# Optimization experiments

Measured on AMD Instinct MI355X. Metric: run time of the kernel, lower is better.

The kernel has to match this reference:

```python
import jax, jax.numpy as jnp
import numpy as np

BS, C_IN, CTX, TGT = 2, 8, 1024, 96
D_MODEL, N_HEADS, D_FF, N_LAYERS = 256, 16, 1024, 4
PF, SF, PC, SC = 8, 4, 32, 16
NF = (CTX + SF - PF) // SF + 1   # 256 fine patches (incl. end-pad)
NC = (CTX + SC - PC) // SC + 1   # 64 coarse patches
TOTAL = NF + NC                  # 320
EPS = 1e-5
DK = D_MODEL // N_HEADS
SCALE = DK ** -0.5


def _patchify(z, plen, stride):
    # ReplicationPad1d((0, stride)) then unfold -> (bs, c, n_patches, plen)
    pad = jnp.broadcast_to(z[..., -1:], z.shape[:-1] + (stride,))
    zp = jnp.concatenate([z, pad], axis=-1)
    n = (zp.shape[-1] - plen) // stride + 1
    idx = np.arange(n)[:, None] * stride + np.arange(plen)[None, :]
    return zp[..., idx]


def _layernorm(x, s, b):
    m = x.mean(-1, keepdims=True)
    v = jnp.var(x, axis=-1, keepdims=True)
    return (x - m) * jax.lax.rsqrt(v + EPS) * s + b


def setup_inputs() -> dict:
    key = jax.random.key(0)
    ks = jax.random.split(key, 16)
    g = lambda k, shape: jax.random.normal(k, shape, jnp.float32) * 0.02
    return {
        "z": jax.random.normal(ks[0], (BS, C_IN, CTX), jnp.float32),
        "revin_w": jnp.ones((C_IN,), jnp.float32),
        "revin_b": jnp.zeros((C_IN,), jnp.float32),
        "Wf": g(ks[1], (PF, D_MODEL)), "bf": jnp.zeros((D_MODEL,), jnp.float32),
        "Wc": g(ks[2], (PC, D_MODEL)), "bc": jnp.zeros((D_MODEL,), jnp.float32),
        "W_pos": jax.random.uniform(ks[3], (TOTAL, D_MODEL), jnp.float32, -0.02, 0.02),
        "WQ": g(ks[4], (N_LAYERS, D_MODEL, D_MODEL)), "bQ": jnp.zeros((N_LAYERS, D_MODEL), jnp.float32),
        "WK": g(ks[5], (N_LAYERS, D_MODEL, D_MODEL)), "bK": jnp.zeros((N_LAYERS, D_MODEL), jnp.float32),
        "WV": g(ks[6], (N_LAYERS, D_MODEL, D_MODEL)), "bV": jnp.zeros((N_LAYERS, D_MODEL), jnp.float32),
        "WO": g(ks[7], (N_LAYERS, D_MODEL, D_MODEL)), "bO": jnp.zeros((N_LAYERS, D_MODEL), jnp.float32),
        "ln1_s": jnp.ones((N_LAYERS, D_MODEL), jnp.float32), "ln1_b": jnp.zeros((N_LAYERS, D_MODEL), jnp.float32),
        "ln2_s": jnp.ones((N_LAYERS, D_MODEL), jnp.float32), "ln2_b": jnp.zeros((N_LAYERS, D_MODEL), jnp.float32),
        "F1": g(ks[8], (N_LAYERS, D_MODEL, D_FF)), "c1": jnp.zeros((N_LAYERS, D_FF), jnp.float32),
        "F2": g(ks[9], (N_LAYERS, D_FF, D_MODEL)), "c2": jnp.zeros((N_LAYERS, D_MODEL), jnp.float32),
        "Wh": g(ks[10], (D_MODEL * TOTAL, TGT)), "bh": jnp.zeros((TGT,), jnp.float32),
    }


def reference(z, revin_w, revin_b, Wf, bf, Wc, bc, W_pos, WQ, bQ, WK, bK, WV, bV,
              WO, bO, ln1_s, ln1_b, ln2_s, ln2_b, F1, c1, F2, c2, Wh, bh):
    # RevIN norm over the time axis (last axis of (bs, c, T))
    mean = z.mean(-1, keepdims=True)
    std = jnp.sqrt(jnp.var(z, axis=-1, keepdims=True) + EPS)
    zn = (z - mean) / std * revin_w[None, :, None] + revin_b[None, :, None]

    # dual-scale patch embedding
    x_fine = _patchify(zn, PF, SF) @ Wf + bf      # (bs, c, NF, d)
    x_coarse = _patchify(zn, PC, SC) @ Wc + bc    # (bs, c, NC, d)
    x = jnp.concatenate([x_fine, x_coarse], axis=2)  # (bs, c, TOTAL, d)

    u = x.reshape(BS * C_IN, TOTAL, D_MODEL) + W_pos  # (B, S, d), B=bs*c

    # residual-score transformer encoder (post-norm)
    prev = None
    for l in range(N_LAYERS):
        q = (u @ WQ[l] + bQ[l]).reshape(-1, TOTAL, N_HEADS, DK).transpose(0, 2, 1, 3)
        k = (u @ WK[l] + bK[l]).reshape(-1, TOTAL, N_HEADS, DK).transpose(0, 2, 1, 3)
        v = (u @ WV[l] + bV[l]).reshape(-1, TOTAL, N_HEADS, DK).transpose(0, 2, 1, 3)
        s = jnp.einsum('bhqd,bhkd->bhqk', q, k) * SCALE
        if prev is not None:
            s = s + prev
        w = jax.nn.softmax(s, axis=-1)
        o = jnp.einsum('bhqk,bhkd->bhqd', w, v).transpose(0, 2, 1, 3).reshape(-1, TOTAL, D_MODEL)
        o = o @ WO[l] + bO[l]
        u = _layernorm(u + o, ln1_s[l], ln1_b[l])
        h = jax.nn.gelu(u @ F1[l] + c1[l], approximate=False) @ F2[l] + c2[l]
        u = _layernorm(u + h, ln2_s[l], ln2_b[l])
        prev = s

    # head: (bs, c, TOTAL, d) -> permute -> flatten(d, TOTAL) -> linear
    zz = u.reshape(BS, C_IN, TOTAL, D_MODEL).transpose(0, 1, 3, 2).reshape(BS, C_IN, D_MODEL * TOTAL)
    out = zz @ Wh + bh  # (bs, c, TGT)

    # RevIN denorm
    out = (out - revin_b[None, :, None]) / (revin_w[None, :, None] + EPS * EPS) * std + mean
    return out
```

## Files before the change

kernel.cpp:

```cpp
#include <hip/hip_runtime.h>
#include <math.h>

typedef unsigned short ushort;
typedef unsigned int uint;
typedef __attribute__((ext_vector_type(8))) short short8;
typedef __attribute__((ext_vector_type(4))) float f32x4;
typedef __attribute__((ext_vector_type(4))) ushort us4;

constexpr int BS = 2, C_IN = 8, CTX = 1024, TGT = 96;
constexpr int DM = 256, NH = 16, DFF = 1024, NL = 4;
constexpr int NF = 256, TOTAL = 320;
constexpr int NB = 16;
constexpr int DK = 16;
constexpr float EPS = 1e-5f;
constexpr float SCALE = 0.25f;
constexpr int KHEAD = DM * TOTAL;
constexpr int M = NB * TOTAL;

__device__ __forceinline__ ushort f2b(float x) {
    uint u = __float_as_uint(x);
    u += 0x7fff + ((u >> 16) & 1);
    return (ushort)(u >> 16);
}
__device__ __forceinline__ float bu2f(ushort x) { return __uint_as_float(((uint)x) << 16); }
__device__ __forceinline__ uint pack2(float a, float b) { return (uint)f2b(a) | ((uint)f2b(b) << 16); }

typedef __attribute__((address_space(3))) uint lds_u32;
typedef const __attribute__((address_space(1))) uint glb_u32;
__device__ __forceinline__ void ldst16(const void* g, void* l) {
    __builtin_amdgcn_global_load_lds((glb_u32*)g, (lds_u32*)l, 16, 0, 0);
}

#define PIPE_BARRIER() asm volatile("s_waitcnt vmcnt(0)\n\ts_barrier" ::: "memory")

__global__ __launch_bounds__(256) void k_prep(
        const float* __restrict__ WQ, const float* __restrict__ WK,
        const float* __restrict__ WV, const float* __restrict__ WO,
        const float* __restrict__ F1, const float* __restrict__ F2,
        const float* __restrict__ Wh,
        ushort* __restrict__ Wtqkv, ushort* __restrict__ WtO,
        ushort* __restrict__ Ft1, ushort* __restrict__ Ft2,
        ushort* __restrict__ WhT2,
        const float* __restrict__ z, const float* __restrict__ rw,
        const float* __restrict__ rb,
        const float* __restrict__ Wf, const float* __restrict__ bfv,
        const float* __restrict__ Wc, const float* __restrict__ bcv,
        const float* __restrict__ Wpos, ushort* __restrict__ u,
        const float* __restrict__ bhv, float* __restrict__ outp,
        float* __restrict__ scalef) {
    __shared__ __align__(16) ushort tile[64 * 98];
    __shared__ float szn[CTX];
    __shared__ float red1[4], red2[4];
    int i = blockIdx.x, tid = threadIdx.x;

    if (i < 768) {
        const float* src; ushort* dst; int lsrc, ldst_, r0, c0;
        if (i < 256) {
            int mat = i >> 4, l = mat >> 2, w = mat & 3;
            src = (w == 0 ? WQ : (w == 1 ? WK : (w == 2 ? WV : WO))) + l * 65536;
            dst = (w < 3) ? (Wtqkv + (size_t)l * 768 * 256 + w * 65536)
                          : (WtO + (size_t)l * 65536);
            lsrc = 256; ldst_ = 256; r0 = ((i >> 2) & 3) * 64; c0 = (i & 3) * 64;
        } else if (i < 512) {
            int j = i - 256, l = j >> 6, t = j & 63;
            src = F1 + (size_t)l * 262144; dst = Ft1 + (size_t)l * 262144;
            lsrc = 1024; ldst_ = 256; r0 = (t >> 4) * 64; c0 = (t & 15) * 64;
        } else {
            int j = i - 512, l = j >> 6, t = j & 63;
            src = F2 + (size_t)l * 262144; dst = Ft2 + (size_t)l * 262144;
            lsrc = 256; ldst_ = 1024; r0 = (t >> 2) * 64; c0 = (t & 3) * 64;
        }
#pragma unroll
        for (int it = 0; it < 4; it++) {
            int fid = it * 256 + tid;
            int fr = fid >> 4, fc = fid & 15;
            f32x4 v = *(const f32x4*)&src[(size_t)(r0 + fr) * lsrc + c0 + fc * 4];
            ushort* tr = &tile[fr * 66];
            tr[fc * 4 + 0] = f2b(v[0]); tr[fc * 4 + 1] = f2b(v[1]);
            tr[fc * 4 + 2] = f2b(v[2]); tr[fc * 4 + 3] = f2b(v[3]);
        }
        __syncthreads();
#pragma unroll
        for (int it = 0; it < 4; it++) {
            int sid = it * 256 + tid;
            int cr = sid >> 4, cc = sid & 15;
            us4 v = (us4){ tile[(cc * 4 + 0) * 66 + cr], tile[(cc * 4 + 1) * 66 + cr],
                           tile[(cc * 4 + 2) * 66 + cr], tile[(cc * 4 + 3) * 66 + cr] };
            *(us4*)&dst[(size_t)(c0 + cr) * ldst_ + r0 + cc * 4] = v;
        }
    } else if (i < 2048) {
        int j = i - 768;
        int pp = j >> 2, d0 = (j & 3) * 64;
#pragma unroll
        for (int it = 0; it < 6; it++) {
            int fid = it * 256 + tid;
            int fr = fid / 24, fc = fid % 24;
            f32x4 v = *(const f32x4*)&Wh[((size_t)(d0 + fr) * 320 + pp) * 96 + fc * 4];
            ushort* tr = &tile[fr * 98];
            tr[fc * 4 + 0] = f2b(v[0]); tr[fc * 4 + 1] = f2b(v[1]);
            tr[fc * 4 + 2] = f2b(v[2]); tr[fc * 4 + 3] = f2b(v[3]);
        }
        __syncthreads();
#pragma unroll
        for (int it = 0; it < 6; it++) {
            int sid = it * 256 + tid;
            int tr = sid >> 4, dc = sid & 15;
            us4 v = (us4){ tile[(dc * 4 + 0) * 98 + tr], tile[(dc * 4 + 1) * 98 + tr],
                           tile[(dc * 4 + 2) * 98 + tr], tile[(dc * 4 + 3) * 98 + tr] };
            *(us4*)&WhT2[(size_t)tr * KHEAD + pp * 256 + d0 + dc * 4] = v;
        }
    } else {
        int j = i - 2048;
        int bc = j / 80, pb = j % 80;
        int wave = tid >> 6, lane = tid & 63;
        f32x4 zv = *(const f32x4*)&z[bc * CTX + tid * 4];
        float s1 = zv[0] + zv[1] + zv[2] + zv[3];
        float s2 = zv[0] * zv[0] + zv[1] * zv[1] + zv[2] * zv[2] + zv[3] * zv[3];
#pragma unroll
        for (int off = 1; off < 64; off <<= 1) {
            s1 += __shfl_xor(s1, off);
            s2 += __shfl_xor(s2, off);
        }
        if (lane == 0) { red1[wave] = s1; red2[wave] = s2; }
        __syncthreads();
        s1 = red1[0] + red1[1] + red1[2] + red1[3];
        s2 = red2[0] + red2[1] + red2[2] + red2[3];
        float m = s1 * (1.0f / CTX);
        float var = s2 * (1.0f / CTX) - m * m;
        float sd = sqrtf(var + EPS);
        int c = bc & 7;
        float w = rw[c], bb = rb[c];
        float inv_sd_w = w / sd;
#pragma unroll
        for (int k = 0; k < 4; k++) szn[tid * 4 + k] = (zv[k] - m) * inv_sd_w + bb;
        if (pb == 0) {
            if (tid < TGT) outp[bc * TGT + tid] = (bhv[tid] - bb) / (w + EPS * EPS) * sd + m;
            if (tid == 0) scalef[bc] = sd / (w + EPS * EPS);
        }
        __syncthreads();
#pragma unroll
        for (int pi = 0; pi < 4; pi++) {
            int p = pb * 4 + pi, d = tid;
            float acc;
            if (p < NF) {
                acc = bfv[d];
                int base = p * 4;
#pragma unroll
                for (int q = 0; q < 8; q++)
                    acc += szn[min(base + q, CTX - 1)] * Wf[q * DM + d];
            } else {
                acc = bcv[d];
                int base = (p - NF) * 16;
#pragma unroll
                for (int q = 0; q < 32; q++)
                    acc += szn[min(base + q, CTX - 1)] * Wc[q * DM + d];
            }
            acc += Wpos[p * DM + d];
            u[((size_t)bc * TOTAL + p) * DM + d] = f2b(acc);
        }
    }
}

template <int GELU, int QKV>
__global__ __launch_bounds__(256) void k_gemm_mfma(const ushort* __restrict__ A,
                                                   const ushort* __restrict__ Wt,
                                                   const float* __restrict__ b0,
                                                   const float* __restrict__ b1,
                                                   const float* __restrict__ b2,
                                                   ushort* __restrict__ C,
                                                   ushort* __restrict__ C2,
                                                   int Mm, int N, int K) {
    __shared__ ushort As[2][64][32];
    __shared__ ushort Bs[2][64][32];
    int tid = threadIdx.x;
    int wave = tid >> 6, lane = tid & 63;
    int quad = lane >> 4, l16 = lane & 15;
    int m0 = blockIdx.y * 64, n0 = blockIdx.x * 64;

    f32x4 acc[4];
#pragma unroll
    for (int nt = 0; nt < 4; nt++) acc[nt] = (f32x4){0.f, 0.f, 0.f, 0.f};

    int srow = wave * 16 + (lane >> 2);
    int sc = (lane & 3) ^ ((srow >> 1) & 3);
    const ushort* Ag = &A[(size_t)(m0 + srow) * K + sc * 8];
    const ushort* Bg = &Wt[(size_t)(n0 + srow) * K + sc * 8];
    int rchunk = (quad ^ ((l16 >> 1) & 3)) * 8;

    ldst16(Ag, &As[0][wave * 16][0]);
    ldst16(Bg, &Bs[0][wave * 16][0]);
    PIPE_BARRIER();

    int nstep = K >> 5;
    int cur = 0;
    for (int t = 0; t < nstep; t++) {
        if (t + 1 < nstep) {
            ldst16(Ag + (t + 1) * 32, &As[cur ^ 1][wave * 16][0]);
            ldst16(Bg + (t + 1) * 32, &Bs[cur ^ 1][wave * 16][0]);
        }
        short8 af = *(const short8*)&As[cur][wave * 16 + l16][rchunk];
#pragma unroll
        for (int nt = 0; nt < 4; nt++) {
            short8 bf = *(const short8*)&Bs[cur][nt * 16 + l16][rchunk];
            acc[nt] = __builtin_amdgcn_mfma_f32_16x16x32_bf16(af, bf, acc[nt], 0, 0, 0);
        }
        PIPE_BARRIER();
        cur ^= 1;
    }
#pragma unroll
    for (int nt = 0; nt < 4; nt++) {
        int col = n0 + nt * 16 + l16;
        float bi;
        if (QKV) {
            int bs = (n0 + nt * 16) >> 8;
            const float* bp = bs == 0 ? b0 : (bs == 1 ? b1 : b2);
            bi = bp[col & 255];
        } else {
            bi = b0[col];
        }
#pragma unroll
        for (int r = 0; r < 4; r++) {
            int rowm = m0 + wave * 16 + quad * 4 + r;
            float vv = acc[nt][r] + bi;
            if (GELU) vv = vv * 0.5f * (1.0f + erff(vv * 0.70710678118f));
            if (QKV) {
                int bs = col >> 8;
                int c = col & 255, hh = c >> 4, d = c & 15;
                int bb = rowm / 320, j = rowm - bb * 320;
                size_t plane = (size_t)hh * (M * DK) + (size_t)bb * (TOTAL * DK);
                if (bs == 0) {
                    C[plane + (size_t)j * DK + d] = f2b(vv);
                } else if (bs == 1) {
                    int off = (((j >> 4) * 2 + (d >> 3)) * 16 + (j & 15)) * 8 + (d & 7);
                    C[(size_t)M * DM + plane + off] = f2b(vv);
                } else {
                    int off = ((j >> 5) * 4 + ((j & 15) >> 2)) * 128 +
                              (((j >> 4) & 1) << 2) + (j & 3) + d * 8;
                    C2[plane + off] = f2b(vv);
                }
            } else {
                C[(size_t)rowm * N + col] = f2b(vv);
            }
        }
    }
}

__global__ __launch_bounds__(256) void k_gemm_ln16(const ushort* __restrict__ A,
                                                   const ushort* __restrict__ Wt,
                                                   const float* __restrict__ bias,
                                                   const float* __restrict__ ls,
                                                   const float* __restrict__ lb,
                                                   const ushort* __restrict__ ures,
                                                   ushort* __restrict__ uout, int K) {
    __shared__ ushort As[2][16][32];
    __shared__ ushort Bs[2][256][32];
    __shared__ float ps1[16][4], ps2[16][4];
    int tid = threadIdx.x;
    int wave = tid >> 6, lane = tid & 63;
    int quad = lane >> 4, l16 = lane & 15;
    int m0 = blockIdx.x * 16;

    f32x4 acc[4];
#pragma unroll
    for (int nt = 0; nt < 4; nt++) acc[nt] = (f32x4){0.f, 0.f, 0.f, 0.f};

    int brow = wave * 16 + (lane >> 2);
    int bc_swz = (lane & 3) ^ ((brow >> 1) & 3);
    const ushort* Bg0 = &Wt[(size_t)brow * K + bc_swz * 8];
    int ar = lane >> 2;
    int ac = (lane & 3) ^ ((ar >> 1) & 3);
    const ushort* Ag = &A[(size_t)(m0 + ar) * K + ac * 8];
    int rchunk = (quad ^ ((l16 >> 1) & 3)) * 8;

    if (tid < 64) ldst16(Ag, &As[0][0][0]);
#pragma unroll
    for (int i = 0; i < 4; i++)
        ldst16(Bg0 + (size_t)i * 64 * K, &Bs[0][i * 64 + wave * 16][0]);
    PIPE_BARRIER();

    int nstep = K >> 5;
    int cur = 0;
    for (int t = 0; t < nstep; t++) {
        if (t + 1 < nstep) {
            if (tid < 64) ldst16(Ag + (t + 1) * 32, &As[cur ^ 1][0][0]);
#pragma unroll
            for (int i = 0; i < 4; i++)
                ldst16(Bg0 + (size_t)i * 64 * K + (t + 1) * 32, &Bs[cur ^ 1][i * 64 + wave * 16][0]);
        }
        short8 af = *(const short8*)&As[cur][l16][rchunk];
#pragma unroll
        for (int nt = 0; nt < 4; nt++) {
            short8 bf = *(const short8*)&Bs[cur][wave * 64 + nt * 16 + l16][rchunk];
            acc[nt] = __builtin_amdgcn_mfma_f32_16x16x32_bf16(af, bf, acc[nt], 0, 0, 0);
        }
        PIPE_BARRIER();
        cur ^= 1;
    }
    float xv[4][4];
#pragma unroll
    for (int r = 0; r < 4; r++) {
        int rowg = m0 + quad * 4 + r;
        float s1 = 0.f, s2 = 0.f;
#pragma unroll
        for (int nt = 0; nt < 4; nt++) {
            int col = wave * 64 + nt * 16 + l16;
            float x = acc[nt][r] + bias[col] + bu2f(ures[(size_t)rowg * DM + col]);
            xv[r][nt] = x; s1 += x; s2 += x * x;
        }
        s1 += __shfl_xor(s1, 1); s2 += __shfl_xor(s2, 1);
        s1 += __shfl_xor(s1, 2); s2 += __shfl_xor(s2, 2);
        s1 += __shfl_xor(s1, 4); s2 += __shfl_xor(s2, 4);
        s1 += __shfl_xor(s1, 8); s2 += __shfl_xor(s2, 8);
        if (l16 == 0) { ps1[quad * 4 + r][wave] = s1; ps2[quad * 4 + r][wave] = s2; }
    }
    __syncthreads();
#pragma unroll
    for (int r = 0; r < 4; r++) {
        int rowl = quad * 4 + r, rowg = m0 + rowl;
        float s1 = ps1[rowl][0] + ps1[rowl][1] + ps1[rowl][2] + ps1[rowl][3];
        float s2 = ps2[rowl][0] + ps2[rowl][1] + ps2[rowl][2] + ps2[rowl][3];
        float m = s1 * (1.0f / DM);
        float var = s2 * (1.0f / DM) - m * m;
        float rs = rsqrtf(var + EPS);
#pragma unroll
        for (int nt = 0; nt < 4; nt++) {
            int col = wave * 64 + nt * 16 + l16;
            uout[(size_t)rowg * DM + col] = f2b((xv[r][nt] - m) * rs * ls[col] + lb[col]);
        }
    }
}

__global__ __launch_bounds__(256) void k_ffnh(const ushort* __restrict__ u1,
                                              const ushort* __restrict__ F1t,
                                              const ushort* __restrict__ F2t,
                                              const float* __restrict__ c1v,
                                              float* __restrict__ part) {
    __shared__ __align__(16) ushort Au[16 * 256];
    __shared__ ushort Bs[2][256][32];
    __shared__ __align__(16) ushort Hs[16][264];
    int tid = threadIdx.x;
    int wave = tid >> 6, lane = tid & 63;
    int quad = lane >> 4, l16 = lane & 15;
    int m0 = blockIdx.x * 16;
    int half = blockIdx.y;

    int brow = wave * 16 + (lane >> 2);
    int bsw = (lane & 3) ^ ((brow >> 1) & 3);
    int rchunk = (quad ^ ((l16 >> 1) & 3)) * 8;

    {
        int rloc = lane >> 5, k32 = (lane & 31) >> 2, pphys = lane & 3;
#pragma unroll
        for (int s = 0; s < 2; s++) {
            int ci = wave + s * 4;
            int row = 2 * ci + rloc;
            int plog = pphys ^ ((row >> 1) & 3);
            ldst16(&u1[(size_t)(m0 + row) * 256 + k32 * 32 + plog * 8], &Au[ci * 512]);
        }
    }
    PIPE_BARRIER();

    f32x4 acc2[4];
#pragma unroll
    for (int nt = 0; nt < 4; nt++) acc2[nt] = (f32x4){0.f, 0.f, 0.f, 0.f};

    for (int ci = 0; ci < 2; ci++) {
        int c = half * 2 + ci;
        f32x4 acc1[4];
#pragma unroll
        for (int nt = 0; nt < 4; nt++) acc1[nt] = (f32x4){0.f, 0.f, 0.f, 0.f};
        const ushort* Bg1 = &F1t[(size_t)(c * 256 + brow) * 256 + bsw * 8];
#pragma unroll
        for (int i = 0; i < 4; i++) ldst16(Bg1 + (size_t)i * 64 * 256, &Bs[0][i * 64 + wave * 16][0]);
        PIPE_BARRIER();
        int cur = 0;
        for (int t = 0; t < 8; t++) {
            if (t + 1 < 8) {
#pragma unroll
                for (int i = 0; i < 4; i++)
                    ldst16(Bg1 + (size_t)i * 64 * 256 + (t + 1) * 32, &Bs[cur ^ 1][i * 64 + wave * 16][0]);
            }
            short8 af = *(const short8*)&Au[l16 * 256 + t * 32 + rchunk];
#pragma unroll
            for (int nt = 0; nt < 4; nt++) {
                short8 bf = *(const short8*)&Bs[cur][wave * 64 + nt * 16 + l16][rchunk];
                acc1[nt] = __builtin_amdgcn_mfma_f32_16x16x32_bf16(af, bf, acc1[nt], 0, 0, 0);
            }
            PIPE_BARRIER();
            cur ^= 1;
        }
#pragma unroll
        for (int nt = 0; nt < 4; nt++) {
            int cc = wave * 64 + nt * 16 + l16;
            float bi = c1v[c * 256 + cc];
            int k32 = cc >> 5, pp = (cc >> 3) & 3, e = cc & 7;
#pragma unroll
            for (int r = 0; r < 4; r++) {
                int row = quad * 4 + r;
                float vv = acc1[nt][r] + bi;
                vv = vv * 0.5f * (1.0f + erff(vv * 0.70710678118f));
                int pphys = pp ^ ((row >> 1) & 3);
                Hs[row][k32 * 32 + pphys * 8 + e] = f2b(vv);
            }
        }
        __syncthreads();
        const ushort* Bg2 = &F2t[(size_t)brow * 1024 + c * 256 + bsw * 8];
#pragma unroll
        for (int i = 0; i < 4; i++) ldst16(Bg2 + (size_t)i * 64 * 1024, &Bs[0][i * 64 + wave * 16][0]);
        PIPE_BARRIER();
        cur = 0;
        for (int t = 0; t < 8; t++) {
            if (t + 1 < 8) {
#pragma unroll
                for (int i = 0; i < 4; i++)
                    ldst16(Bg2 + (size_t)i * 64 * 1024 + (t + 1) * 32, &Bs[cur ^ 1][i * 64 + wave * 16][0]);
            }
            short8 af = *(const short8*)&Hs[l16][t * 32 + rchunk];
#pragma unroll
            for (int nt = 0; nt < 4; nt++) {
                short8 bf = *(const short8*)&Bs[cur][wave * 64 + nt * 16 + l16][rchunk];
                acc2[nt] = __builtin_amdgcn_mfma_f32_16x16x32_bf16(af, bf, acc2[nt], 0, 0, 0);
            }
            PIPE_BARRIER();
            cur ^= 1;
        }
    }

#pragma unroll
    for (int nt = 0; nt < 4; nt++) {
        int col = wave * 64 + nt * 16 + l16;
#pragma unroll
        for (int r = 0; r < 4; r++) {
            int rowg = m0 + quad * 4 + r;
            part[((size_t)half * M + rowg) * 256 + col] = acc2[nt][r];
        }
    }
}

__global__ __launch_bounds__(256) void k_ln2red(const float* __restrict__ part,
                                                const float* __restrict__ c2v,
                                                const ushort* __restrict__ u1,
                                                const float* __restrict__ ls,
                                                const float* __restrict__ lb,
                                                ushort* __restrict__ u) {
    int tid = threadIdx.x;
    int wave = tid >> 6, lane = tid & 63;
    int m0 = blockIdx.x * 16;
#pragma unroll
    for (int r = 0; r < 4; r++) {
        int row = m0 + wave * 4 + r;
        f32x4 a = *(const f32x4*)&part[(size_t)row * 256 + lane * 4];
        f32x4 b = *(const f32x4*)&part[(size_t)(M + row) * 256 + lane * 4];
        us4 ur = *(const us4*)&u1[(size_t)row * 256 + lane * 4];
        float x[4];
        float s1 = 0.f, s2 = 0.f;
#pragma unroll
        for (int j = 0; j < 4; j++) {
            x[j] = a[j] + b[j] + c2v[lane * 4 + j] + bu2f(ur[j]);
            s1 += x[j]; s2 += x[j] * x[j];
        }
#pragma unroll
        for (int off = 1; off < 64; off <<= 1) {
            s1 += __shfl_xor(s1, off);
            s2 += __shfl_xor(s2, off);
        }
        float m = s1 * (1.0f / DM);
        float var = s2 * (1.0f / DM) - m * m;
        float rs = rsqrtf(var + EPS);
        us4 o;
#pragma unroll
        for (int j = 0; j < 4; j++)
            o[j] = f2b((x[j] - m) * rs * ls[lane * 4 + j] + lb[lane * 4 + j]);
        *(us4*)&u[(size_t)row * 256 + lane * 4] = o;
    }
}

__global__ __launch_bounds__(256, 3) void k_attn(const ushort* __restrict__ qk, const ushort* __restrict__ vm,
                                                 ushort* __restrict__ ao, int nj) {
    __shared__ __align__(16) ushort sh[25600];
    int bh = blockIdx.x, b = bh >> 4, h = bh & 15;
    int i0 = blockIdx.y * 64;
    int t = threadIdx.x, wave = t >> 6, lane = t & 63, quad = lane >> 4, l16 = lane & 15;
    const short8 zero8 = (short8){0, 0, 0, 0, 0, 0, 0, 0};
    size_t hplane = (size_t)h * (M * DK) + (size_t)b * (TOTAL * DK);

    int nchunks = (nj + 1) * 10;
    for (int c = wave; c < nchunks; c += 4) {
        int s = c / 10, cc = c - s * 10;
        const ushort* src = (s < nj)
            ? qk + (size_t)(2 * s + 1) * (M * DM) + hplane + cc * 512
            : vm + hplane + cc * 512;
        int dstbase = (s < nj ? s * 5120 : 20480) + cc * 512;
        ldst16(src + lane * 8, &sh[dstbase]);
    }
    short8 qfr[4] = { zero8, zero8, zero8, zero8 };
    int qrow = i0 + wave * 16 + l16;
#pragma unroll
    for (int jl = 0; jl < 4; jl++)
        if (jl < nj && quad < 2)
            qfr[jl] = *(const short8*)&qk[(size_t)(2 * jl) * (M * DM) + hplane +
                                          (size_t)qrow * DK + quad * 8];
    PIPE_BARRIER();

    f32x4 acc[20];
#pragma unroll
    for (int nt = 0; nt < 20; nt++) acc[nt] = (f32x4){0.f, 0.f, 0.f, 0.f};

    __builtin_amdgcn_s_setprio(1);
#pragma unroll
    for (int jl = 0; jl < 4; jl++) {
        if (jl < nj) {
            int kb = jl * 5120;
#pragma unroll
            for (int nt = 0; nt < 20; nt++) {
                short8 kf = *(const short8*)&sh[kb + ((nt * 2 + (quad & 1)) * 16 + l16) * 8];
                acc[nt] = __builtin_amdgcn_mfma_f32_16x16x32_bf16(kf, qfr[jl], acc[nt], 0, 0, 0);
            }
        }
    }
    __builtin_amdgcn_s_setprio(0);

    float mx = -1e30f;
#pragma unroll
    for (int nt = 0; nt < 20; nt++)
#pragma unroll
        for (int r = 0; r < 4; r++) { acc[nt][r] *= SCALE; mx = fmaxf(mx, acc[nt][r]); }
    mx = fmaxf(mx, __shfl_xor(mx, 16));
    mx = fmaxf(mx, __shfl_xor(mx, 32));
    float sum = 0.f;
#pragma unroll
    for (int nt = 0; nt < 20; nt++)
#pragma unroll
        for (int r = 0; r < 4; r++) { acc[nt][r] = __expf(acc[nt][r] - mx); sum += acc[nt][r]; }
    sum += __shfl_xor(sum, 16);
    sum += __shfl_xor(sum, 32);
    float inv = 1.f / sum;
#pragma unroll
    for (int nt = 0; nt < 20; nt++)
#pragma unroll
        for (int r = 0; r < 4; r++) acc[nt][r] *= inv;

    f32x4 oacc = (f32x4){0.f, 0.f, 0.f, 0.f};
    __builtin_amdgcn_s_setprio(1);
#pragma unroll
    for (int jt2 = 0; jt2 < 10; jt2++) {
        short8 vt = *(const short8*)&sh[20480 + ((jt2 * 4 + quad) * 16 + l16) * 8];
        union { short8 v; uint u[4]; } pf;
        pf.u[0] = pack2(acc[2 * jt2][0], acc[2 * jt2][1]);
        pf.u[1] = pack2(acc[2 * jt2][2], acc[2 * jt2][3]);
        pf.u[2] = pack2(acc[2 * jt2 + 1][0], acc[2 * jt2 + 1][1]);
        pf.u[3] = pack2(acc[2 * jt2 + 1][2], acc[2 * jt2 + 1][3]);
        oacc = __builtin_amdgcn_mfma_f32_16x16x32_bf16(vt, pf.v, oacc, 0, 0, 0);
    }
    __builtin_amdgcn_s_setprio(0);
    us4 ov4 = (us4){f2b(oacc[0]), f2b(oacc[1]), f2b(oacc[2]), f2b(oacc[3])};
    *(us4*)&ao[((size_t)b * TOTAL + i0 + wave * 16 + l16) * DM + h * DK + quad * 4] = ov4;
}

__global__ __launch_bounds__(256) void k_head(const ushort* __restrict__ u, const ushort* __restrict__ WhT2,
                                              const float* __restrict__ scalef, float* __restrict__ out) {
    int t0 = blockIdx.x * 16;
    int wave = threadIdx.x >> 6, lane = threadIdx.x & 63;
    int quad = lane >> 4, l16 = lane & 15;
    int chunk = blockIdx.y * 4 + wave;
    int kbeg = chunk * 1024;
    f32x4 acc = (f32x4){0.f, 0.f, 0.f, 0.f};
    const ushort* za = &u[(size_t)l16 * KHEAD + quad * 8];
    const ushort* wb = &WhT2[(size_t)(t0 + l16) * KHEAD + quad * 8];
#pragma unroll 4
    for (int k = kbeg; k < kbeg + 1024; k += 32) {
        short8 af = *(const short8*)&za[k];
        short8 bf = *(const short8*)&wb[k];
        acc = __builtin_amdgcn_mfma_f32_16x16x32_bf16(af, bf, acc, 0, 0, 0);
    }
#pragma unroll
    for (int r = 0; r < 4; r++) {
        int bcr = quad * 4 + r;
        atomicAdd(&out[bcr * TGT + t0 + l16], acc[r] * scalef[bcr]);
    }
}

extern "C" void kernel_launch(void* const* d_in, const int* in_sizes, int n_in,
                              void* d_out, int out_size, void* d_ws, size_t ws_size,
                              hipStream_t stream) {
    const float* z       = (const float*)d_in[0];
    const float* revin_w = (const float*)d_in[1];
    const float* revin_b = (const float*)d_in[2];
    const float* Wf      = (const float*)d_in[3];
    const float* bfv     = (const float*)d_in[4];
    const float* Wc      = (const float*)d_in[5];
    const float* bcv     = (const float*)d_in[6];
    const float* Wpos    = (const float*)d_in[7];
    const float* WQ      = (const float*)d_in[8];
    const float* bQ      = (const float*)d_in[9];
    const float* WK      = (const float*)d_in[10];
    const float* bK      = (const float*)d_in[11];
    const float* WV      = (const float*)d_in[12];
    const float* bV      = (const float*)d_in[13];
    const float* WO      = (const float*)d_in[14];
    const float* bO      = (const float*)d_in[15];
    const float* ln1s    = (const float*)d_in[16];
    const float* ln1b    = (const float*)d_in[17];
    const float* ln2s    = (const float*)d_in[18];
    const float* ln2b    = (const float*)d_in[19];
    const float* F1      = (const float*)d_in[20];
    const float* c1      = (const float*)d_in[21];
    const float* F2      = (const float*)d_in[22];
    const float* c2      = (const float*)d_in[23];
    const float* Wh      = (const float*)d_in[24];
    const float* bh      = (const float*)d_in[25];
    float* out = (float*)d_out;

    char* p = (char*)d_ws;
    float* scalef = (float*)p;   p += 16 * 4;
    p = (char*)(((size_t)p + 255) & ~255ull);
    ushort* u     = (ushort*)p;  p += (size_t)M * DM * 2;
    ushort* u1    = (ushort*)p;  p += (size_t)M * DM * 2;
    ushort* qkbuf = (ushort*)p;  p += (size_t)NL * 2 * M * DM * 2;
    ushort* vbuf  = (ushort*)p;  p += (size_t)M * DM * 2;
    ushort* ax    = (ushort*)p;  p += (size_t)M * DM * 2;
    float* part   = (float*)p;   p += (size_t)2 * M * 256 * 4;
    ushort* Wtqkv = (ushort*)p;  p += (size_t)NL * 768 * 256 * 2;
    ushort* WtO   = (ushort*)p;  p += (size_t)NL * 256 * 256 * 2;
    ushort* Ft1   = (ushort*)p;  p += (size_t)NL * 1024 * 256 * 2;
    ushort* Ft2   = (ushort*)p;  p += (size_t)NL * 256 * 1024 * 2;
    ushort* WhT2  = (ushort*)p;  p += (size_t)TGT * KHEAD * 2;

    k_prep<<<3328, 256, 0, stream>>>(WQ, WK, WV, WO, F1, F2, Wh,
                                     Wtqkv, WtO, Ft1, Ft2, WhT2,
                                     z, revin_w, revin_b,
                                     Wf, bfv, Wc, bcv, Wpos, u,
                                     bh, out, scalef);

    for (int l = 0; l < NL; l++) {
        k_gemm_mfma<0, 1><<<dim3(12, 80), 256, 0, stream>>>(
            u, Wtqkv + (size_t)l * 768 * 256, bQ + l * DM, bK + l * DM, bV + l * DM,
            qkbuf + (size_t)l * 2 * M * DM, vbuf, M, 768, 256);
        k_attn<<<dim3(NB * NH, 5), 256, 0, stream>>>(qkbuf, vbuf, ax, l + 1);
        k_gemm_ln16<<<M / 16, 256, 0, stream>>>(
            ax, WtO + (size_t)l * 65536, bO + l * DM, ln1s + l * DM, ln1b + l * DM,
            u, u1, 256);
        k_ffnh<<<dim3(M / 16, 2), 256, 0, stream>>>(
            u1, Ft1 + (size_t)l * 262144, Ft2 + (size_t)l * 262144, c1 + l * DFF, part);
        k_ln2red<<<M / 16, 256, 0, stream>>>(
            part, c2 + l * DM, u1, ln2s + l * DM, ln2b + l * DM, u);
    }

    k_head<<<dim3(TGT / 16, 20), 256, 0, stream>>>(u, WhT2, scalef, out);
}
```

Before: 409.6 us.

## Fuse FFN halves and LN2 into one kernel with fragment-packed weights

```diff
diff --git a/kernel.cpp b/kernel.cpp
--- a/kernel.cpp
+++ b/kernel.cpp
@@ -53,28 +53,17 @@
     __shared__ float red1[4], red2[4];
     int i = blockIdx.x, tid = threadIdx.x;
 
-    if (i < 768) {
-        const float* src; ushort* dst; int lsrc, ldst_, r0, c0;
-        if (i < 256) {
-            int mat = i >> 4, l = mat >> 2, w = mat & 3;
-            src = (w == 0 ? WQ : (w == 1 ? WK : (w == 2 ? WV : WO))) + l * 65536;
-            dst = (w < 3) ? (Wtqkv + (size_t)l * 768 * 256 + w * 65536)
-                          : (WtO + (size_t)l * 65536);
-            lsrc = 256; ldst_ = 256; r0 = ((i >> 2) & 3) * 64; c0 = (i & 3) * 64;
-        } else if (i < 512) {
-            int j = i - 256, l = j >> 6, t = j & 63;
-            src = F1 + (size_t)l * 262144; dst = Ft1 + (size_t)l * 262144;
-            lsrc = 1024; ldst_ = 256; r0 = (t >> 4) * 64; c0 = (t & 15) * 64;
-        } else {
-            int j = i - 512, l = j >> 6, t = j & 63;
-            src = F2 + (size_t)l * 262144; dst = Ft2 + (size_t)l * 262144;
-            lsrc = 256; ldst_ = 1024; r0 = (t >> 2) * 64; c0 = (t & 3) * 64;
-        }
+    if (i < 256) {
+        int mat = i >> 4, l = mat >> 2, w = mat & 3;
+        const float* src = (w == 0 ? WQ : (w == 1 ? WK : (w == 2 ? WV : WO))) + l * 65536;
+        ushort* dst = (w < 3) ? (Wtqkv + (size_t)l * 768 * 256 + w * 65536)
+                              : (WtO + (size_t)l * 65536);
+        int r0 = ((i >> 2) & 3) * 64, c0 = (i & 3) * 64;
 #pragma unroll
         for (int it = 0; it < 4; it++) {
             int fid = it * 256 + tid;
             int fr = fid >> 4, fc = fid & 15;
-            f32x4 v = *(const f32x4*)&src[(size_t)(r0 + fr) * lsrc + c0 + fc * 4];
+            f32x4 v = *(const f32x4*)&src[(size_t)(r0 + fr) * 256 + c0 + fc * 4];
             ushort* tr = &tile[fr * 66];
             tr[fc * 4 + 0] = f2b(v[0]); tr[fc * 4 + 1] = f2b(v[1]);
             tr[fc * 4 + 2] = f2b(v[2]); tr[fc * 4 + 3] = f2b(v[3]);
@@ -86,7 +75,57 @@
             int cr = sid >> 4, cc = sid & 15;
             us4 v = (us4){ tile[(cc * 4 + 0) * 66 + cr], tile[(cc * 4 + 1) * 66 + cr],
                            tile[(cc * 4 + 2) * 66 + cr], tile[(cc * 4 + 3) * 66 + cr] };
-            *(us4*)&dst[(size_t)(c0 + cr) * ldst_ + r0 + cc * 4] = v;
+            *(us4*)&dst[(size_t)(c0 + cr) * 256 + r0 + cc * 4] = v;
+        }
+    } else if (i < 512) {
+        int j = i - 256, l = j >> 6, t = j & 63;
+        const float* src = F1 + (size_t)l * 262144;
+        ushort* dst = Ft1 + (size_t)l * 262144;
+        int r0 = (t >> 4) * 64, c0 = (t & 15) * 64;
+#pragma unroll
+        for (int it = 0; it < 4; it++) {
+            int fid = it * 256 + tid;
+            int fr = fid >> 4, fc = fid & 15;
+            f32x4 v = *(const f32x4*)&src[(size_t)(r0 + fr) * 1024 + c0 + fc * 4];
+            ushort* tr = &tile[fr * 66];
+            tr[fc * 4 + 0] = f2b(v[0]); tr[fc * 4 + 1] = f2b(v[1]);
+            tr[fc * 4 + 2] = f2b(v[2]); tr[fc * 4 + 3] = f2b(v[3]);
+        }
+        __syncthreads();
+#pragma unroll
+        for (int it = 0; it < 4; it++) {
+            int sid = it * 256 + tid;
+            int nl = sid >> 4, e4 = sid & 15;
+            int kl = e4 * 4;
+            int kcg = (r0 + kl) >> 5, e = kl & 31;
+            us4 v = (us4){ tile[(kl + 0) * 66 + nl], tile[(kl + 1) * 66 + nl],
+                           tile[(kl + 2) * 66 + nl], tile[(kl + 3) * 66 + nl] };
+            *(us4*)&dst[((size_t)kcg * 1024 + c0 + nl) * 32 + e] = v;
+        }
+    } else if (i < 768) {
+        int j = i - 512, l = j >> 6, t = j & 63;
+        const float* src = F2 + (size_t)l * 262144;
+        ushort* dst = Ft2 + (size_t)l * 262144;
+        int r0 = (t >> 2) * 64, c0 = (t & 3) * 64;
+#pragma unroll
+        for (int it = 0; it < 4; it++) {
+            int fid = it * 256 + tid;
+            int fr = fid >> 4, fc = fid & 15;
+            f32x4 v = *(const f32x4*)&src[(size_t)(r0 + fr) * 256 + c0 + fc * 4];
+            ushort* tr = &tile[fr * 66];
+            tr[fc * 4 + 0] = f2b(v[0]); tr[fc * 4 + 1] = f2b(v[1]);
+            tr[fc * 4 + 2] = f2b(v[2]); tr[fc * 4 + 3] = f2b(v[3]);
+        }
+        __syncthreads();
+#pragma unroll
+        for (int it = 0; it < 4; it++) {
+            int sid = it * 256 + tid;
+            int nl = sid >> 4, e4 = sid & 15;
+            int kl = e4 * 4;
+            int kcg = (r0 + kl) >> 5, e = kl & 31;
+            us4 v = (us4){ tile[(kl + 0) * 66 + nl], tile[(kl + 1) * 66 + nl],
+                           tile[(kl + 2) * 66 + nl], tile[(kl + 3) * 66 + nl] };
+            *(us4*)&dst[((size_t)kcg * 256 + c0 + nl) * 32 + e] = v;
         }
     } else if (i < 2048) {
         int j = i - 768;
@@ -330,22 +369,21 @@
     }
 }
 
-__global__ __launch_bounds__(256) void k_ffnh(const ushort* __restrict__ u1,
-                                              const ushort* __restrict__ F1t,
-                                              const ushort* __restrict__ F2t,
+__global__ __launch_bounds__(256) void k_ffn3(const ushort* __restrict__ u1,
+                                              const ushort* __restrict__ Ft1b,
+                                              const ushort* __restrict__ Ft2b,
                                               const float* __restrict__ c1v,
-                                              float* __restrict__ part) {
+                                              const float* __restrict__ c2v,
+                                              const float* __restrict__ ls,
+                                              const float* __restrict__ lb,
+                                              ushort* __restrict__ u) {
     __shared__ __align__(16) ushort Au[16 * 256];
-    __shared__ ushort Bs[2][256][32];
     __shared__ __align__(16) ushort Hs[16][264];
+    __shared__ float ps1[16][4], ps2[16][4];
     int tid = threadIdx.x;
     int wave = tid >> 6, lane = tid & 63;
     int quad = lane >> 4, l16 = lane & 15;
     int m0 = blockIdx.x * 16;
-    int half = blockIdx.y;
-
-    int brow = wave * 16 + (lane >> 2);
-    int bsw = (lane & 3) ^ ((brow >> 1) & 3);
     int rchunk = (quad ^ ((l16 >> 1) & 3)) * 8;
 
     {
@@ -364,31 +402,21 @@
 #pragma unroll
     for (int nt = 0; nt < 4; nt++) acc2[nt] = (f32x4){0.f, 0.f, 0.f, 0.f};
 
-    for (int ci = 0; ci < 2; ci++) {
-        int c = half * 2 + ci;
+    for (int c = 0; c < 4; c++) {
         f32x4 acc1[4];
 #pragma unroll
         for (int nt = 0; nt < 4; nt++) acc1[nt] = (f32x4){0.f, 0.f, 0.f, 0.f};
-        const ushort* Bg1 = &F1t[(size_t)(c * 256 + brow) * 256 + bsw * 8];
-#pragma unroll
-        for (int i = 0; i < 4; i++) ldst16(Bg1 + (size_t)i * 64 * 256, &Bs[0][i * 64 + wave * 16][0]);
-        PIPE_BARRIER();
-        int cur = 0;
+#pragma unroll
         for (int t = 0; t < 8; t++) {
-            if (t + 1 < 8) {
-#pragma unroll
-                for (int i = 0; i < 4; i++)
-                    ldst16(Bg1 + (size_t)i * 64 * 256 + (t + 1) * 32, &Bs[cur ^ 1][i * 64 + wave * 16][0]);
-            }
             short8 af = *(const short8*)&Au[l16 * 256 + t * 32 + rchunk];
 #pragma unroll
             for (int nt = 0; nt < 4; nt++) {
-                short8 bf = *(const short8*)&Bs[cur][wave * 64 + nt * 16 + l16][rchunk];
+                int coln = c * 256 + wave * 64 + nt * 16 + l16;
+                short8 bf = *(const short8*)&Ft1b[((size_t)t * 1024 + coln) * 32 + quad * 8];
                 acc1[nt] = __builtin_amdgcn_mfma_f32_16x16x32_bf16(af, bf, acc1[nt], 0, 0, 0);
             }
-            PIPE_BARRIER();
-            cur ^= 1;
-        }
+        }
+        if (c > 0) __syncthreads();
 #pragma unroll
         for (int nt = 0; nt < 4; nt++) {
             int cc = wave * 64 + nt * 16 + l16;
@@ -404,74 +432,51 @@
             }
         }
         __syncthreads();
-        const ushort* Bg2 = &F2t[(size_t)brow * 1024 + c * 256 + bsw * 8];
-#pragma unroll
-        for (int i = 0; i < 4; i++) ldst16(Bg2 + (size_t)i * 64 * 1024, &Bs[0][i * 64 + wave * 16][0]);
-        PIPE_BARRIER();
-        cur = 0;
+#pragma unroll
         for (int t = 0; t < 8; t++) {
-            if (t + 1 < 8) {
-#pragma unroll
-                for (int i = 0; i < 4; i++)
-                    ldst16(Bg2 + (size_t)i * 64 * 1024 + (t + 1) * 32, &Bs[cur ^ 1][i * 64 + wave * 16][0]);
-            }
             short8 af = *(const short8*)&Hs[l16][t * 32 + rchunk];
 #pragma unroll
             for (int nt = 0; nt < 4; nt++) {
-                short8 bf = *(const short8*)&Bs[cur][wave * 64 + nt * 16 + l16][rchunk];
+                int n = wave * 64 + nt * 16 + l16;
+                short8 bf = *(const short8*)&Ft2b[((size_t)(c * 8 + t) * 256 + n) * 32 + quad * 8];
                 acc2[nt] = __builtin_amdgcn_mfma_f32_16x16x32_bf16(af, bf, acc2[nt], 0, 0, 0);
             }
-            PIPE_BARRIER();
-            cur ^= 1;
-        }
-    }
-
-#pragma unroll
-    for (int nt = 0; nt < 4; nt++) {
-        int col = wave * 64 + nt * 16 + l16;
-#pragma unroll
-        for (int r = 0; r < 4; r++) {
-            int rowg = m0 + quad * 4 + r;
-            part[((size_t)half * M + rowg) * 256 + col] = acc2[nt][r];
-        }
-    }
-}
-
-__global__ __launch_bounds__(256) void k_ln2red(const float* __restrict__ part,
-                                                const float* __restrict__ c2v,
-                                                const ushort* __restrict__ u1,
-                                                const float* __restrict__ ls,
-                                                const float* __restrict__ lb,
-                                                ushort* __restrict__ u) {
-    int tid = threadIdx.x;
-    int wave = tid >> 6, lane = tid & 63;
-    int m0 = blockIdx.x * 16;
+        }
+    }
+
+    float xv[4][4];
 #pragma unroll
     for (int r = 0; r < 4; r++) {
-        int row = m0 + wave * 4 + r;
-        f32x4 a = *(const f32x4*)&part[(size_t)row * 256 + lane * 4];
-        f32x4 b = *(const f32x4*)&part[(size_t)(M + row) * 256 + lane * 4];
-        us4 ur = *(const us4*)&u1[(size_t)row * 256 + lane * 4];
-        float x[4];
+        int rowl = quad * 4 + r;
         float s1 = 0.f, s2 = 0.f;
 #pragma unroll
-        for (int j = 0; j < 4; j++) {
-            x[j] = a[j] + b[j] + c2v[lane * 4 + j] + bu2f(ur[j]);
-            s1 += x[j]; s2 += x[j] * x[j];
-        }
-#pragma unroll
-        for (int off = 1; off < 64; off <<= 1) {
-            s1 += __shfl_xor(s1, off);
-            s2 += __shfl_xor(s2, off);
-        }
+        for (int nt = 0; nt < 4; nt++) {
+            int col = wave * 64 + nt * 16 + l16;
+            int k32 = col >> 5, pp = (col >> 3) & 3, e = col & 7;
+            int pphys = pp ^ ((rowl >> 1) & 3);
+            float x = acc2[nt][r] + c2v[col] + bu2f(Au[rowl * 256 + k32 * 32 + pphys * 8 + e]);
+            xv[r][nt] = x; s1 += x; s2 += x * x;
+        }
+        s1 += __shfl_xor(s1, 1); s2 += __shfl_xor(s2, 1);
+        s1 += __shfl_xor(s1, 2); s2 += __shfl_xor(s2, 2);
+        s1 += __shfl_xor(s1, 4); s2 += __shfl_xor(s2, 4);
+        s1 += __shfl_xor(s1, 8); s2 += __shfl_xor(s2, 8);
+        if (l16 == 0) { ps1[rowl][wave] = s1; ps2[rowl][wave] = s2; }
+    }
+    __syncthreads();
+#pragma unroll
+    for (int r = 0; r < 4; r++) {
+        int rowl = quad * 4 + r, rowg = m0 + rowl;
+        float s1 = ps1[rowl][0] + ps1[rowl][1] + ps1[rowl][2] + ps1[rowl][3];
+        float s2 = ps2[rowl][0] + ps2[rowl][1] + ps2[rowl][2] + ps2[rowl][3];
         float m = s1 * (1.0f / DM);
         float var = s2 * (1.0f / DM) - m * m;
         float rs = rsqrtf(var + EPS);
-        us4 o;
-#pragma unroll
-        for (int j = 0; j < 4; j++)
-            o[j] = f2b((x[j] - m) * rs * ls[lane * 4 + j] + lb[lane * 4 + j]);
-        *(us4*)&u[(size_t)row * 256 + lane * 4] = o;
+#pragma unroll
+        for (int nt = 0; nt < 4; nt++) {
+            int col = wave * 64 + nt * 16 + l16;
+            u[(size_t)rowg * DM + col] = f2b((xv[r][nt] - m) * rs * ls[col] + lb[col]);
+        }
     }
 }
 
@@ -619,7 +624,6 @@
     ushort* qkbuf = (ushort*)p;  p += (size_t)NL * 2 * M * DM * 2;
     ushort* vbuf  = (ushort*)p;  p += (size_t)M * DM * 2;
     ushort* ax    = (ushort*)p;  p += (size_t)M * DM * 2;
-    float* part   = (float*)p;   p += (size_t)2 * M * 256 * 4;
     ushort* Wtqkv = (ushort*)p;  p += (size_t)NL * 768 * 256 * 2;
     ushort* WtO   = (ushort*)p;  p += (size_t)NL * 256 * 256 * 2;
     ushort* Ft1   = (ushort*)p;  p += (size_t)NL * 1024 * 256 * 2;
@@ -640,10 +644,9 @@
         k_gemm_ln16<<<M / 16, 256, 0, stream>>>(
             ax, WtO + (size_t)l * 65536, bO + l * DM, ln1s + l * DM, ln1b + l * DM,
             u, u1, 256);
-        k_ffnh<<<dim3(M / 16, 2), 256, 0, stream>>>(
-            u1, Ft1 + (size_t)l * 262144, Ft2 + (size_t)l * 262144, c1 + l * DFF, part);
-        k_ln2red<<<M / 16, 256, 0, stream>>>(
-            part, c2 + l * DM, u1, ln2s + l * DM, ln2b + l * DM, u);
+        k_ffn3<<<M / 16, 256, 0, stream>>>(
+            u1, Ft1 + (size_t)l * 262144, Ft2 + (size_t)l * 262144,
+            c1 + l * DFF, c2 + l * DM, ln2s + l * DM, ln2b + l * DM, u);
     }
 
     k_head<<<dim3(TGT / 16, 20), 256, 0, stream>>>(u, WhT2, scalef, out);
```

Measured after the change: 427.7 us. 1.04x slower.
